# Performance work log

Measured on AMD Instinct MI355X. Metric: run time of the kernel, lower is better.

The kernel has to match this reference:

```python
import jax, jax.numpy as jnp
import numpy as np

N, E, D, H, C = 100000, 1600000, 128, 256, 40


def setup_inputs() -> dict:
    key = jax.random.key(0)
    ks = jax.random.split(key, 10)
    x = jax.random.normal(ks[0], (N, D), dtype=jnp.float32)
    src = jax.random.randint(ks[1], (E,), 0, N, dtype=jnp.int32)
    dst = jax.random.randint(ks[2], (E,), 0, N, dtype=jnp.int32)
    # GIN layer 1 MLP (bias-free), kaiming-uniform-like scale 1/sqrt(fan_in)
    w1a = jax.random.normal(ks[3], (D, H), dtype=jnp.float32) / np.sqrt(D)
    w1b = jax.random.normal(ks[4], (H, H), dtype=jnp.float32) / np.sqrt(H)
    # GIN layer 2 MLP
    w2a = jax.random.normal(ks[5], (H, H), dtype=jnp.float32) / np.sqrt(H)
    w2b = jax.random.normal(ks[6], (H, H), dtype=jnp.float32) / np.sqrt(H)
    # eps initialized to 0 per reset_parameters
    eps1 = jnp.zeros((), dtype=jnp.float32)
    eps2 = jnp.zeros((), dtype=jnp.float32)
    # final classifier fc (with bias)
    fc_w = jax.random.normal(ks[7], (H, C), dtype=jnp.float32) / np.sqrt(H)
    fc_b = jax.random.normal(ks[8], (C,), dtype=jnp.float32) * 0.01
    return {"x": x, "src": src, "dst": dst,
            "eps1": eps1, "w1a": w1a, "w1b": w1b,
            "eps2": eps2, "w2a": w2a, "w2b": w2b,
            "fc_w": fc_w, "fc_b": fc_b}


def reference(x, src, dst, eps1, w1a, w1b, eps2, w2a, w2b, fc_w, fc_b):
    n = x.shape[0]

    def gin_layer(h, eps, wa, wb):
        # GINConv sum-aggregation: scatter-add neighbor feats over edges
        agg = jax.ops.segment_sum(h[src], dst, num_segments=n)  # [N, d]
        rst = (1.0 + eps) * h + agg
        # 2-layer bias-free MLP with ReLU between
        return jax.nn.relu(rst @ wa) @ wb

    h = jax.nn.relu(gin_layer(x, eps1, w1a, w1b))   # layer + outer activation
    h = jax.nn.relu(gin_layer(h, eps2, w2a, w2b))   # dropout p=0 -> identity
    return h @ fc_w + fc_b                           # [N, C]
```

## Files before the change

### kernel.cpp

```cpp
#include <hip/hip_runtime.h>

#define N_NODES 100000
#define N_EDGES 1600000
#define DIM_IN  128
#define DIM_H   256
#define DIM_C   40

#define NB   391
#define NBLK 391
#define CHUNK 4096
#define ECAP 6144

typedef unsigned short bf16_t;
typedef __attribute__((ext_vector_type(8))) short short8;
typedef __attribute__((ext_vector_type(4))) float f32x4;

__device__ __forceinline__ bf16_t f2b(float f) {
    unsigned int u = __float_as_uint(f);
    unsigned int r = (u + 0x7fffu + ((u >> 16) & 1u)) >> 16;
    return (bf16_t)r;
}
__device__ __forceinline__ float b2f(unsigned int h16) {
    return __uint_as_float(h16 << 16);
}

__device__ __forceinline__ void gl_lds16(const void* gsrc, void* ldst) {
    __builtin_amdgcn_global_load_lds(
        (const __attribute__((address_space(1))) void*)gsrc,
        (__attribute__((address_space(3))) void*)ldst,
        16, 0, 0);
}


__global__ void k_bhist(const int* __restrict__ dst, int* __restrict__ cnt2, int e) {
    __shared__ int h[NB];
    int t = threadIdx.x, blk = blockIdx.x;
    for (int i = t; i < NB; i += 256) h[i] = 0;
    __syncthreads();
    int base = blk * CHUNK;
    int end = min(base + CHUNK, e);
    for (int i = base + t; i < end; i += 256)
        atomicAdd(&h[dst[i] >> 8], 1);
    __syncthreads();
    for (int i = t; i < NB; i += 256) cnt2[blk * NB + i] = h[i];
}

__global__ void k_bscanA(const int* __restrict__ cnt2, int* __restrict__ basep,
                         int* __restrict__ btot) {
    __shared__ int s[512];
    int t = threadIdx.x, b = blockIdx.x;
    int v = (t < NBLK) ? cnt2[t * NB + b] : 0;
    s[t] = v;
    __syncthreads();
    #pragma unroll
    for (int d = 1; d < 512; d <<= 1) {
        int tv = (t >= d) ? s[t - d] : 0;
        __syncthreads();
        s[t] += tv;
        __syncthreads();
    }
    if (t < NBLK) basep[t * NB + b] = s[t] - v;
    if (t == 511) btot[b] = s[511];
}

__global__ void k_bscan2(const int* __restrict__ btot, int* __restrict__ boff) {
    __shared__ int s[512];
    int t = threadIdx.x;
    int v = (t < NB) ? btot[t] : 0;
    s[t] = v;
    __syncthreads();
    #pragma unroll
    for (int d = 1; d < 512; d <<= 1) {
        int tv = (t >= d) ? s[t - d] : 0;
        __syncthreads();
        s[t] += tv;
        __syncthreads();
    }
    if (t < NB) boff[t] = s[t] - v;
    if (t == NB - 1) boff[NB] = s[t];
}

__global__ void k_bscatter(const int* __restrict__ src, const int* __restrict__ dst,
                           const int* __restrict__ basep, const int* __restrict__ boff,
                           int2* __restrict__ ebuf, int e) {
    __shared__ int cur[NB];
    int t = threadIdx.x, blk = blockIdx.x;
    for (int i = t; i < NB; i += 256) cur[i] = basep[blk * NB + i] + boff[i];
    __syncthreads();
    int base = blk * CHUNK;
    int end = min(base + CHUNK, e);
    for (int i = base + t; i < end; i += 256) {
        int sv = src[i], dv = dst[i];
        int pos = atomicAdd(&cur[dv >> 8], 1);
        ebuf[pos] = make_int2(sv, dv);
    }
}

__global__ __launch_bounds__(256) void k_build(const int2* __restrict__ ebuf,
                                               const int* __restrict__ boff,
                                               int* __restrict__ off,
                                               int* __restrict__ csr) {
    __shared__ int2 ec[ECAP];
    __shared__ int h[256];
    __shared__ int cur[256];
    int t = threadIdx.x, b = blockIdx.x;
    int node0 = b << 8;
    int e0 = boff[b], e1 = boff[b + 1];
    int ne = e1 - e0;
    bool fits = (ne <= ECAP);
    h[t] = 0;
    __syncthreads();
    if (fits) {
        for (int i = t; i < ne; i += 256) {
            int2 p = ebuf[e0 + i];
            ec[i] = p;
            atomicAdd(&h[p.y - node0], 1);
        }
    } else {
        for (int i = t; i < ne; i += 256)
            atomicAdd(&h[ebuf[e0 + i].y - node0], 1);
    }
    __syncthreads();
    int mydeg = h[t];
    #pragma unroll
    for (int d = 1; d < 256; d <<= 1) {
        int tv = (t >= d) ? h[t - d] : 0;
        __syncthreads();
        h[t] += tv;
        __syncthreads();
    }
    int node = node0 + t;
    if (node < N_NODES) off[node + 1] = e0 + h[t];
    if (b == 0 && t == 0) off[0] = 0;
    cur[t] = e0 + h[t] - mydeg;
    __syncthreads();
    if (fits) {
        for (int i = t; i < ne; i += 256) {
            int2 p = ec[i];
            int pos = atomicAdd(&cur[p.y - node0], 1);
            csr[pos] = p.x;
        }
    } else {
        for (int i = t; i < ne; i += 256) {
            int2 p = ebuf[e0 + i];
            int pos = atomicAdd(&cur[p.y - node0], 1);
            csr[pos] = p.x;
        }
    }
}


__global__ void k_cvt4(const float* __restrict__ in, bf16_t* __restrict__ out, int n4) {
    int i = blockIdx.x * 256 + threadIdx.x;
    if (i < n4) {
        float4 v = ((const float4*)in)[i];
        ushort4 o;
        o.x = f2b(v.x); o.y = f2b(v.y); o.z = f2b(v.z); o.w = f2b(v.w);
        ((ushort4*)out)[i] = o;
    }
}

__global__ void k_wcvt(const float* __restrict__ w1a, const float* __restrict__ w1b,
                       const float* __restrict__ w2a, const float* __restrict__ w2b,
                       const float* __restrict__ fcw,
                       bf16_t* __restrict__ o1a, bf16_t* __restrict__ o1b,
                       bf16_t* __restrict__ o2a, bf16_t* __restrict__ o2b,
                       bf16_t* __restrict__ ofc) {
    int r = blockIdx.y;
    int idx = blockIdx.x * 256 + threadIdx.x;
    const float* in; bf16_t* out; int K, N, Npad;
    switch (r) {
        case 0: in = w1a; out = o1a; K = 128; N = 256; Npad = 256; break;
        case 1: in = w1b; out = o1b; K = 256; N = 256; Npad = 256; break;
        case 2: in = w2a; out = o2a; K = 256; N = 256; Npad = 256; break;
        case 3: in = w2b; out = o2b; K = 256; N = 256; Npad = 256; break;
        default: in = fcw; out = ofc; K = 256; N = 40;  Npad = 128; break;
    }
    if (idx >= Npad * K) return;
    int n = idx / K, k = idx - n * K;
    float v = (n < N) ? in[(size_t)k * N + n] : 0.f;
    out[idx] = f2b(v);
}


template <int D>
__global__ void k_agg_b(const bf16_t* __restrict__ h, const int* __restrict__ off,
                        const int* __restrict__ csr, const float* __restrict__ eps_p,
                        bf16_t* __restrict__ rst, int n) {
    constexpr int V = D / 64;
    int gid = blockIdx.x * blockDim.x + threadIdx.x;
    int u = gid >> 6;
    int lane = gid & 63;
    if (u >= n) return;

    float acc[V];
    #pragma unroll
    for (int j = 0; j < V; j++) acc[j] = 0.f;

    int r0 = off[u], r1 = off[u + 1];
    int r = r0;
    for (; r + 8 <= r1; r += 8) {
        int s[8];
        #pragma unroll
        for (int t = 0; t < 8; t++) s[t] = csr[r + t];
        unsigned int v[8];
        #pragma unroll
        for (int t = 0; t < 8; t++)
            v[t] = *(const unsigned int*)(h + (size_t)s[t] * D + lane * 2);
        #pragma unroll
        for (int t = 0; t < 8; t++) {
            acc[0] += b2f(v[t] & 0xffffu);
            acc[1] += b2f(v[t] >> 16);
        }
    }
    for (; r < r1; r++) {
        int s = csr[r];
        unsigned int v = *(const unsigned int*)(h + (size_t)s * D + lane * 2);
        acc[0] += b2f(v & 0xffffu);
        acc[1] += b2f(v >> 16);
    }

    float ep = 1.0f + eps_p[0];
    unsigned int v = *(const unsigned int*)(h + (size_t)u * D + lane * 2);
    float o0 = ep * b2f(v & 0xffffu) + acc[0];
    float o1 = ep * b2f(v >> 16) + acc[1];
    *(unsigned int*)(rst + (size_t)u * D + lane * 2) =
        (unsigned int)f2b(o0) | ((unsigned int)f2b(o1) << 16);
}


__global__ void k_agg_u8(const unsigned char* __restrict__ h8,
                         const float* __restrict__ hs,
                         const int* __restrict__ off, const int* __restrict__ csr,
                         const float* __restrict__ eps_p,
                         bf16_t* __restrict__ rst, int n) {
    int gid = blockIdx.x * blockDim.x + threadIdx.x;
    int u = gid >> 6;
    int lane = gid & 63;
    if (u >= n) return;

    float acc[4] = {0.f, 0.f, 0.f, 0.f};
    int r0 = off[u], r1 = off[u + 1];
    int r = r0;
    for (; r + 8 <= r1; r += 8) {
        int s[8];
        #pragma unroll
        for (int t = 0; t < 8; t++) s[t] = csr[r + t];
        unsigned int v[8];
        float sc[8];
        #pragma unroll
        for (int t = 0; t < 8; t++) {
            v[t] = *(const unsigned int*)(h8 + (size_t)s[t] * 256 + lane * 4);
            sc[t] = hs[s[t]];
        }
        #pragma unroll
        for (int t = 0; t < 8; t++) {
            acc[0] += (float)(v[t] & 0xffu) * sc[t];
            acc[1] += (float)((v[t] >> 8) & 0xffu) * sc[t];
            acc[2] += (float)((v[t] >> 16) & 0xffu) * sc[t];
            acc[3] += (float)(v[t] >> 24) * sc[t];
        }
    }
    for (; r < r1; r++) {
        int s = csr[r];
        unsigned int v = *(const unsigned int*)(h8 + (size_t)s * 256 + lane * 4);
        float sc = hs[s];
        acc[0] += (float)(v & 0xffu) * sc;
        acc[1] += (float)((v >> 8) & 0xffu) * sc;
        acc[2] += (float)((v >> 16) & 0xffu) * sc;
        acc[3] += (float)(v >> 24) * sc;
    }

    float ep = 1.0f + eps_p[0];
    unsigned int vu = *(const unsigned int*)(h8 + (size_t)u * 256 + lane * 4);
    float scu = hs[u] * ep;
    float o0 = (float)(vu & 0xffu) * scu + acc[0];
    float o1 = (float)((vu >> 8) & 0xffu) * scu + acc[1];
    float o2 = (float)((vu >> 16) & 0xffu) * scu + acc[2];
    float o3 = (float)(vu >> 24) * scu + acc[3];
    uint2 ov;
    ov.x = (unsigned int)f2b(o0) | ((unsigned int)f2b(o1) << 16);
    ov.y = (unsigned int)f2b(o2) | ((unsigned int)f2b(o3) << 16);
    *(uint2*)(rst + (size_t)u * 256 + lane * 4) = ov;
}


#define TS_STRIDE 264

template <int K1, bool OUT8>
__global__ __launch_bounds__(256, 2) void k_mlp(
    const bf16_t* __restrict__ A, const bf16_t* __restrict__ W1t,
    const bf16_t* __restrict__ W2t, bf16_t* __restrict__ H,
    unsigned char* __restrict__ H8, float* __restrict__ Hs, int M)
{
    __shared__ __align__(16) bf16_t As[64 * 32];
    __shared__ __align__(16) bf16_t Bs[256 * 32];
    __shared__ __align__(16) bf16_t Ts[64 * TS_STRIDE];
    __shared__ int rmax[64];

    int tid = threadIdx.x;
    int wave = tid >> 6, lane = tid & 63;
    int l15 = lane & 15, quad = lane >> 4;
    int bm = blockIdx.x * 64;
    int wn = wave * 64;

    f32x4 acc[4][4];
    #pragma unroll
    for (int i = 0; i < 4; i++)
        #pragma unroll
        for (int j = 0; j < 4; j++) acc[i][j] = 0.f;

    for (int k0 = 0; k0 < K1; k0 += 32) {
        {
            int row = tid >> 2, k8 = (tid & 3) * 8;
            int gr = bm + row; if (gr >= M) gr = M - 1;
            gl_lds16(A + (size_t)gr * K1 + k0 + k8, &As[(wave * 64) * 8]);
        }
        #pragma unroll
        for (int l = 0; l < 4; l++) {
            int s = l * 256 + tid;
            int row = s >> 2, k8 = (s & 3) * 8;
            gl_lds16(W1t + (size_t)row * K1 + k0 + k8, &Bs[(size_t)(l * 256 + wave * 64) * 8]);
        }
        __syncthreads();

        short8 af[4], bfv[4];
        #pragma unroll
        for (int i = 0; i < 4; i++)
            af[i] = *(const short8*)&As[(i * 16 + l15) * 32 + quad * 8];
        #pragma unroll
        for (int j = 0; j < 4; j++)
            bfv[j] = *(const short8*)&Bs[(wn + j * 16 + l15) * 32 + quad * 8];

        #pragma unroll
        for (int i = 0; i < 4; i++)
            #pragma unroll
            for (int j = 0; j < 4; j++)
                acc[i][j] = __builtin_amdgcn_mfma_f32_16x16x32_bf16(af[i], bfv[j], acc[i][j], 0, 0, 0);
        __syncthreads();
    }

    #pragma unroll
    for (int i = 0; i < 4; i++)
        #pragma unroll
        for (int j = 0; j < 4; j++) {
            int row = i * 16 + quad * 4;
            int col = wn + j * 16 + l15;
            #pragma unroll
            for (int r = 0; r < 4; r++)
                Ts[(row + r) * TS_STRIDE + col] = f2b(fmaxf(acc[i][j][r], 0.f));
        }

    #pragma unroll
    for (int i = 0; i < 4; i++)
        #pragma unroll
        for (int j = 0; j < 4; j++) acc[i][j] = 0.f;
    __syncthreads();

    for (int k0 = 0; k0 < 256; k0 += 32) {
        #pragma unroll
        for (int l = 0; l < 4; l++) {
            int s = l * 256 + tid;
            int row = s >> 2, k8 = (s & 3) * 8;
            gl_lds16(W2t + (size_t)row * 256 + k0 + k8, &Bs[(size_t)(l * 256 + wave * 64) * 8]);
        }
        __syncthreads();

        short8 af[4], bfv[4];
        #pragma unroll
        for (int i = 0; i < 4; i++)
            af[i] = *(const short8*)&Ts[(i * 16 + l15) * TS_STRIDE + k0 + quad * 8];
        #pragma unroll
        for (int j = 0; j < 4; j++)
            bfv[j] = *(const short8*)&Bs[(wn + j * 16 + l15) * 32 + quad * 8];

        #pragma unroll
        for (int i = 0; i < 4; i++)
            #pragma unroll
            for (int j = 0; j < 4; j++)
                acc[i][j] = __builtin_amdgcn_mfma_f32_16x16x32_bf16(af[i], bfv[j], acc[i][j], 0, 0, 0);
        __syncthreads();
    }

    if constexpr (OUT8) {
        if (tid < 64) rmax[tid] = 0;
        __syncthreads();
        #pragma unroll
        for (int i = 0; i < 4; i++)
            #pragma unroll
            for (int r = 0; r < 4; r++) {
                float m = 0.f;
                #pragma unroll
                for (int j = 0; j < 4; j++) m = fmaxf(m, acc[i][j][r]);
                atomicMax(&rmax[i * 16 + quad * 4 + r], __float_as_int(m));
            }
        __syncthreads();
        #pragma unroll
        for (int i = 0; i < 4; i++) {
            #pragma unroll
            for (int r = 0; r < 4; r++) {
                int row = i * 16 + quad * 4 + r;
                int rowg = bm + row;
                if (rowg >= M) continue;
                float rm = __int_as_float(rmax[row]);
                float inv = (rm > 0.f) ? 255.f / rm : 0.f;
                #pragma unroll
                for (int j = 0; j < 4; j++) {
                    int col = wn + j * 16 + l15;
                    float v = fmaxf(acc[i][j][r], 0.f);
                    unsigned q = (unsigned)(v * inv + 0.5f);
                    if (q > 255u) q = 255u;
                    H8[(size_t)rowg * 256 + col] = (unsigned char)q;
                }
                if (wave == 0 && l15 == 0)
                    Hs[rowg] = rm * (1.f / 255.f);
            }
        }
    } else {
        #pragma unroll
        for (int j = 0; j < 4; j++) {
            int col = wn + j * 16 + l15;
            #pragma unroll
            for (int i = 0; i < 4; i++) {
                #pragma unroll
                for (int r = 0; r < 4; r++) {
                    int rowg = bm + i * 16 + quad * 4 + r;
                    if (rowg < M)
                        H[(size_t)rowg * 256 + col] = f2b(fmaxf(acc[i][j][r], 0.f));
                }
            }
        }
    }
}


__global__ __launch_bounds__(256) void gemm_fc(
    const bf16_t* __restrict__ A, const bf16_t* __restrict__ Bt,
    const float* __restrict__ bias, float* __restrict__ C,
    int M, int K, int Nst)
{
    __shared__ __align__(16) bf16_t As[128 * 32];
    __shared__ __align__(16) bf16_t Bs[128 * 32];

    int tid = threadIdx.x;
    int wave = tid >> 6, lane = tid & 63;
    int l15 = lane & 15, quad = lane >> 4;
    int bm = blockIdx.y * 128, bn = blockIdx.x * 128;
    int wm = (wave >> 1) * 64, wn = (wave & 1) * 64;

    f32x4 acc[4][4];
    #pragma unroll
    for (int i = 0; i < 4; i++)
        #pragma unroll
        for (int j = 0; j < 4; j++) acc[i][j] = 0.f;

    for (int k0 = 0; k0 < K; k0 += 32) {
        #pragma unroll
        for (int iss = 0; iss < 2; iss++) {
            int s = iss * 256 + wave * 64 + lane;
            int row = s >> 2;
            int k8 = (s & 3) * 8;
            int ldsoff = (iss * 256 + wave * 64) * 8;

            int grA = bm + row; if (grA >= M) grA = M - 1;
            gl_lds16(A + (size_t)grA * K + k0 + k8, &As[ldsoff]);

            int grB = bn + row;
            gl_lds16(Bt + (size_t)grB * K + k0 + k8, &Bs[ldsoff]);
        }
        __syncthreads();

        short8 af[4], bfv[4];
        #pragma unroll
        for (int i = 0; i < 4; i++)
            af[i] = *(const short8*)&As[(wm + i * 16 + l15) * 32 + quad * 8];
        #pragma unroll
        for (int j = 0; j < 4; j++)
            bfv[j] = *(const short8*)&Bs[(wn + j * 16 + l15) * 32 + quad * 8];

        #pragma unroll
        for (int i = 0; i < 4; i++)
            #pragma unroll
            for (int j = 0; j < 4; j++)
                acc[i][j] = __builtin_amdgcn_mfma_f32_16x16x32_bf16(af[i], bfv[j], acc[i][j], 0, 0, 0);
        __syncthreads();
    }

    #pragma unroll
    for (int j = 0; j < 4; j++) {
        int col = bn + wn + j * 16 + l15;
        if (col >= Nst) continue;
        float bv = bias[col];
        #pragma unroll
        for (int i = 0; i < 4; i++) {
            #pragma unroll
            for (int r = 0; r < 4; r++) {
                int rowg = bm + wm + i * 16 + quad * 4 + r;
                if (rowg < M)
                    C[(size_t)rowg * Nst + col] = acc[i][j][r] + bv;
            }
        }
    }
}


static inline size_t rnd256(size_t x) { return (x + 255) & ~(size_t)255; }

extern "C" void kernel_launch(void* const* d_in, const int* in_sizes, int n_in,
                              void* d_out, int out_size, void* d_ws, size_t ws_size,
                              hipStream_t stream) {
    const float* x    = (const float*)d_in[0];
    const int*   src  = (const int*)d_in[1];
    const int*   dst  = (const int*)d_in[2];
    const float* eps1 = (const float*)d_in[3];
    const float* w1a  = (const float*)d_in[4];
    const float* w1b  = (const float*)d_in[5];
    const float* eps2 = (const float*)d_in[6];
    const float* w2a  = (const float*)d_in[7];
    const float* w2b  = (const float*)d_in[8];
    const float* fc_w = (const float*)d_in[9];
    const float* fc_b = (const float*)d_in[10];
    float* out = (float*)d_out;

    char* w = (char*)d_ws;
    int* off  = (int*)w; w += rnd256(sizeof(int) * (size_t)(N_NODES + 1));
    int* csr  = (int*)w; w += rnd256(sizeof(int) * (size_t)N_EDGES);
    int* cnt2  = (int*)w; w += rnd256(sizeof(int) * (size_t)NBLK * NB);
    int* basep = (int*)w; w += rnd256(sizeof(int) * (size_t)NBLK * NB);
    int* btot  = (int*)w; w += rnd256(sizeof(int) * 512);
    int* boff  = (int*)w; w += rnd256(sizeof(int) * (NB + 1));
    bf16_t* w1a_t = (bf16_t*)w; w += rnd256(2 * (size_t)DIM_H * DIM_IN);
    bf16_t* w1b_t = (bf16_t*)w; w += rnd256(2 * (size_t)DIM_H * DIM_H);
    bf16_t* w2a_t = (bf16_t*)w; w += rnd256(2 * (size_t)DIM_H * DIM_H);
    bf16_t* w2b_t = (bf16_t*)w; w += rnd256(2 * (size_t)DIM_H * DIM_H);
    bf16_t* fc_t  = (bf16_t*)w; w += rnd256(2 * (size_t)128 * DIM_H);
    unsigned char* h8 = (unsigned char*)w; w += rnd256((size_t)N_NODES * DIM_H);
    float* hs = (float*)w; w += rnd256(sizeof(float) * (size_t)N_NODES);
    bf16_t* R12 = (bf16_t*)w; w += rnd256(2 * (size_t)N_NODES * DIM_H);
    bf16_t* R3  = (bf16_t*)w; w += rnd256(2 * (size_t)N_NODES * DIM_H);

    bf16_t* xb   = R12;
    bf16_t* rst1 = R12 + (size_t)N_NODES * DIM_IN;
    int2* ebuf = (int2*)R3;

    k_bhist<<<NBLK, 256, 0, stream>>>(dst, cnt2, N_EDGES);
    k_bscanA<<<NB, 512, 0, stream>>>(cnt2, basep, btot);
    k_bscan2<<<1, 512, 0, stream>>>(btot, boff);
    k_bscatter<<<NBLK, 256, 0, stream>>>(src, dst, basep, boff, ebuf, N_EDGES);
    k_build<<<NB, 256, 0, stream>>>(ebuf, boff, off, csr);

    k_cvt4<<<(N_NODES * DIM_IN / 4 + 255) / 256, 256, 0, stream>>>(x, xb, N_NODES * DIM_IN / 4);
    {
        dim3 g(256, 5);
        k_wcvt<<<g, 256, 0, stream>>>(w1a, w1b, w2a, w2b, fc_w,
                                      w1a_t, w1b_t, w2a_t, w2b_t, fc_t);
    }

    const int agg_blocks = (N_NODES * 64 + 255) / 256;
    const int mlp_blocks = (N_NODES + 63) / 64;

    k_agg_b<DIM_IN><<<agg_blocks, 256, 0, stream>>>(xb, off, csr, eps1, rst1, N_NODES);
    k_mlp<DIM_IN, true><<<mlp_blocks, 256, 0, stream>>>(rst1, w1a_t, w1b_t,
                                                        nullptr, h8, hs, N_NODES);

    k_agg_u8<<<agg_blocks, 256, 0, stream>>>(h8, hs, off, csr, eps2, (bf16_t*)R3, N_NODES);
    k_mlp<DIM_H, false><<<mlp_blocks, 256, 0, stream>>>((bf16_t*)R3, w2a_t, w2b_t,
                                                        R12, nullptr, nullptr, N_NODES);

    dim3 g1(1, (N_NODES + 127) / 128);
    gemm_fc<<<g1, 256, 0, stream>>>(R12, fc_t, fc_b, out, N_NODES, DIM_H, DIM_C);
}
```

Baseline: 464.8 us.

## Quantize input features to per-row int8 and pack edge buffer into 32-bit words

The input x is now quantized to int8 with one scale per row instead of bf16, which halves the bytes gathered per edge in the first aggregation. The edge scatter buffer now packs src and the low 8 bits of dst into a single 32-bit int instead of an int2, halving the edge-buffer traffic in scatter and build. The aggregation kernels use 32-bit unsigned address arithmetic. The cost is extra quantization error on the raw input features, and the packing assumes node ids fit in 24 bits.

```diff
diff --git a/kernel.cpp b/kernel.cpp
--- a/kernel.cpp
+++ b/kernel.cpp
@@ -82,7 +82,7 @@
 
 __global__ void k_bscatter(const int* __restrict__ src, const int* __restrict__ dst,
                            const int* __restrict__ basep, const int* __restrict__ boff,
-                           int2* __restrict__ ebuf, int e) {
+                           int* __restrict__ ebuf, int e) {
     __shared__ int cur[NB];
     int t = threadIdx.x, blk = blockIdx.x;
     for (int i = t; i < NB; i += 256) cur[i] = basep[blk * NB + i] + boff[i];
@@ -92,15 +92,15 @@
     for (int i = base + t; i < end; i += 256) {
         int sv = src[i], dv = dst[i];
         int pos = atomicAdd(&cur[dv >> 8], 1);
-        ebuf[pos] = make_int2(sv, dv);
-    }
-}
-
-__global__ __launch_bounds__(256) void k_build(const int2* __restrict__ ebuf,
+        ebuf[pos] = sv | ((dv & 255) << 24);
+    }
+}
+
+__global__ __launch_bounds__(256) void k_build(const int* __restrict__ ebuf,
                                                const int* __restrict__ boff,
                                                int* __restrict__ off,
                                                int* __restrict__ csr) {
-    __shared__ int2 ec[ECAP];
+    __shared__ int ec[ECAP];
     __shared__ int h[256];
     __shared__ int cur[256];
     int t = threadIdx.x, b = blockIdx.x;
@@ -112,13 +112,13 @@
     __syncthreads();
     if (fits) {
         for (int i = t; i < ne; i += 256) {
-            int2 p = ebuf[e0 + i];
+            int p = ebuf[e0 + i];
             ec[i] = p;
-            atomicAdd(&h[p.y - node0], 1);
+            atomicAdd(&h[(unsigned)p >> 24], 1);
         }
     } else {
         for (int i = t; i < ne; i += 256)
-            atomicAdd(&h[ebuf[e0 + i].y - node0], 1);
+            atomicAdd(&h[(unsigned)ebuf[e0 + i] >> 24], 1);
     }
     __syncthreads();
     int mydeg = h[t];
@@ -136,28 +136,36 @@
     __syncthreads();
     if (fits) {
         for (int i = t; i < ne; i += 256) {
-            int2 p = ec[i];
-            int pos = atomicAdd(&cur[p.y - node0], 1);
-            csr[pos] = p.x;
+            int p = ec[i];
+            int pos = atomicAdd(&cur[(unsigned)p >> 24], 1);
+            csr[pos] = p & 0xFFFFFF;
         }
     } else {
         for (int i = t; i < ne; i += 256) {
-            int2 p = ebuf[e0 + i];
-            int pos = atomicAdd(&cur[p.y - node0], 1);
-            csr[pos] = p.x;
-        }
-    }
-}
-
-
-__global__ void k_cvt4(const float* __restrict__ in, bf16_t* __restrict__ out, int n4) {
-    int i = blockIdx.x * 256 + threadIdx.x;
-    if (i < n4) {
-        float4 v = ((const float4*)in)[i];
-        ushort4 o;
-        o.x = f2b(v.x); o.y = f2b(v.y); o.z = f2b(v.z); o.w = f2b(v.w);
-        ((ushort4*)out)[i] = o;
-    }
+            int p = ebuf[e0 + i];
+            int pos = atomicAdd(&cur[(unsigned)p >> 24], 1);
+            csr[pos] = p & 0xFFFFFF;
+        }
+    }
+}
+
+
+__global__ void k_cvt_i8(const float* __restrict__ x, signed char* __restrict__ x8,
+                         float* __restrict__ xs, int n) {
+    int gid = blockIdx.x * blockDim.x + threadIdx.x;
+    int u = gid >> 6, lane = gid & 63;
+    if (u >= n) return;
+    float2 v = *(const float2*)(x + (size_t)u * 128 + lane * 2);
+    float m = fmaxf(fabsf(v.x), fabsf(v.y));
+    #pragma unroll
+    for (int d = 1; d < 64; d <<= 1)
+        m = fmaxf(m, __shfl_xor(m, d, 64));
+    float inv = (m > 0.f) ? 127.f / m : 0.f;
+    int q0 = (int)rintf(v.x * inv);
+    int q1 = (int)rintf(v.y * inv);
+    unsigned short pk = (unsigned short)((q0 & 0xff) | ((q1 & 0xff) << 8));
+    *(unsigned short*)(x8 + ((unsigned)u << 7) + lane * 2) = pk;
+    if (lane == 0) xs[u] = (m > 0.f) ? m * (1.f / 127.f) : 0.f;
 }
 
 __global__ void k_wcvt(const float* __restrict__ w1a, const float* __restrict__ w1b,
@@ -183,48 +191,49 @@
 }
 
 
-template <int D>
-__global__ void k_agg_b(const bf16_t* __restrict__ h, const int* __restrict__ off,
-                        const int* __restrict__ csr, const float* __restrict__ eps_p,
-                        bf16_t* __restrict__ rst, int n) {
-    constexpr int V = D / 64;
+__global__ void k_agg_i8(const signed char* __restrict__ h8, const float* __restrict__ hs,
+                         const int* __restrict__ off, const int* __restrict__ csr,
+                         const float* __restrict__ eps_p,
+                         bf16_t* __restrict__ rst, int n) {
     int gid = blockIdx.x * blockDim.x + threadIdx.x;
     int u = gid >> 6;
     int lane = gid & 63;
     if (u >= n) return;
 
-    float acc[V];
-    #pragma unroll
-    for (int j = 0; j < V; j++) acc[j] = 0.f;
-
+    float acc0 = 0.f, acc1 = 0.f;
     int r0 = off[u], r1 = off[u + 1];
     int r = r0;
+    unsigned loff = lane * 2u;
     for (; r + 8 <= r1; r += 8) {
         int s[8];
         #pragma unroll
         for (int t = 0; t < 8; t++) s[t] = csr[r + t];
-        unsigned int v[8];
-        #pragma unroll
-        for (int t = 0; t < 8; t++)
-            v[t] = *(const unsigned int*)(h + (size_t)s[t] * D + lane * 2);
+        unsigned v[8];
+        float sc[8];
         #pragma unroll
         for (int t = 0; t < 8; t++) {
-            acc[0] += b2f(v[t] & 0xffffu);
-            acc[1] += b2f(v[t] >> 16);
+            v[t] = *(const unsigned short*)(h8 + (((unsigned)s[t] << 7) + loff));
+            sc[t] = hs[s[t]];
+        }
+        #pragma unroll
+        for (int t = 0; t < 8; t++) {
+            acc0 += (float)(int)(signed char)(v[t] & 0xffu) * sc[t];
+            acc1 += (float)(int)(signed char)(v[t] >> 8) * sc[t];
         }
     }
     for (; r < r1; r++) {
         int s = csr[r];
-        unsigned int v = *(const unsigned int*)(h + (size_t)s * D + lane * 2);
-        acc[0] += b2f(v & 0xffffu);
-        acc[1] += b2f(v >> 16);
-    }
-
-    float ep = 1.0f + eps_p[0];
-    unsigned int v = *(const unsigned int*)(h + (size_t)u * D + lane * 2);
-    float o0 = ep * b2f(v & 0xffffu) + acc[0];
-    float o1 = ep * b2f(v >> 16) + acc[1];
-    *(unsigned int*)(rst + (size_t)u * D + lane * 2) =
+        unsigned v = *(const unsigned short*)(h8 + (((unsigned)s << 7) + loff));
+        float sc = hs[s];
+        acc0 += (float)(int)(signed char)(v & 0xffu) * sc;
+        acc1 += (float)(int)(signed char)(v >> 8) * sc;
+    }
+
+    float scu = hs[u] * (1.0f + eps_p[0]);
+    unsigned vu = *(const unsigned short*)(h8 + (((unsigned)u << 7) + loff));
+    float o0 = (float)(int)(signed char)(vu & 0xffu) * scu + acc0;
+    float o1 = (float)(int)(signed char)(vu >> 8) * scu + acc1;
+    *(unsigned int*)(rst + ((unsigned)u << 7) + lane * 2) =
         (unsigned int)f2b(o0) | ((unsigned int)f2b(o1) << 16);
 }
 
@@ -242,6 +251,7 @@
     float acc[4] = {0.f, 0.f, 0.f, 0.f};
     int r0 = off[u], r1 = off[u + 1];
     int r = r0;
+    unsigned loff = lane * 4u;
     for (; r + 8 <= r1; r += 8) {
         int s[8];
         #pragma unroll
@@ -250,7 +260,7 @@
         float sc[8];
         #pragma unroll
         for (int t = 0; t < 8; t++) {
-            v[t] = *(const unsigned int*)(h8 + (size_t)s[t] * 256 + lane * 4);
+            v[t] = *(const unsigned int*)(h8 + (((unsigned)s[t] << 8) + loff));
             sc[t] = hs[s[t]];
         }
         #pragma unroll
@@ -263,7 +273,7 @@
     }
     for (; r < r1; r++) {
         int s = csr[r];
-        unsigned int v = *(const unsigned int*)(h8 + (size_t)s * 256 + lane * 4);
+        unsigned int v = *(const unsigned int*)(h8 + (((unsigned)s << 8) + loff));
         float sc = hs[s];
         acc[0] += (float)(v & 0xffu) * sc;
         acc[1] += (float)((v >> 8) & 0xffu) * sc;
@@ -272,7 +282,7 @@
     }
 
     float ep = 1.0f + eps_p[0];
-    unsigned int vu = *(const unsigned int*)(h8 + (size_t)u * 256 + lane * 4);
+    unsigned int vu = *(const unsigned int*)(h8 + (((unsigned)u << 8) + loff));
     float scu = hs[u] * ep;
     float o0 = (float)(vu & 0xffu) * scu + acc[0];
     float o1 = (float)((vu >> 8) & 0xffu) * scu + acc[1];
@@ -534,14 +544,15 @@
     bf16_t* w2a_t = (bf16_t*)w; w += rnd256(2 * (size_t)DIM_H * DIM_H);
     bf16_t* w2b_t = (bf16_t*)w; w += rnd256(2 * (size_t)DIM_H * DIM_H);
     bf16_t* fc_t  = (bf16_t*)w; w += rnd256(2 * (size_t)128 * DIM_H);
+    signed char* x8 = (signed char*)w; w += rnd256((size_t)N_NODES * DIM_IN);
+    float* xs = (float*)w; w += rnd256(sizeof(float) * (size_t)N_NODES);
     unsigned char* h8 = (unsigned char*)w; w += rnd256((size_t)N_NODES * DIM_H);
     float* hs = (float*)w; w += rnd256(sizeof(float) * (size_t)N_NODES);
     bf16_t* R12 = (bf16_t*)w; w += rnd256(2 * (size_t)N_NODES * DIM_H);
     bf16_t* R3  = (bf16_t*)w; w += rnd256(2 * (size_t)N_NODES * DIM_H);
 
-    bf16_t* xb   = R12;
-    bf16_t* rst1 = R12 + (size_t)N_NODES * DIM_IN;
-    int2* ebuf = (int2*)R3;
+    bf16_t* rst1 = R12;
+    int* ebuf = (int*)R3;
 
     k_bhist<<<NBLK, 256, 0, stream>>>(dst, cnt2, N_EDGES);
     k_bscanA<<<NB, 512, 0, stream>>>(cnt2, basep, btot);
@@ -549,7 +560,7 @@
     k_bscatter<<<NBLK, 256, 0, stream>>>(src, dst, basep, boff, ebuf, N_EDGES);
     k_build<<<NB, 256, 0, stream>>>(ebuf, boff, off, csr);
 
-    k_cvt4<<<(N_NODES * DIM_IN / 4 + 255) / 256, 256, 0, stream>>>(x, xb, N_NODES * DIM_IN / 4);
+    k_cvt_i8<<<(N_NODES * 64 + 255) / 256, 256, 0, stream>>>(x, x8, xs, N_NODES);
     {
         dim3 g(256, 5);
         k_wcvt<<<g, 256, 0, stream>>>(w1a, w1b, w2a, w2b, fc_w,
@@ -559,7 +570,7 @@
     const int agg_blocks = (N_NODES * 64 + 255) / 256;
     const int mlp_blocks = (N_NODES + 63) / 64;
 
-    k_agg_b<DIM_IN><<<agg_blocks, 256, 0, stream>>>(xb, off, csr, eps1, rst1, N_NODES);
+    k_agg_i8<<<agg_blocks, 256, 0, stream>>>(x8, xs, off, csr, eps1, rst1, N_NODES);
     k_mlp<DIM_IN, true><<<mlp_blocks, 256, 0, stream>>>(rst1, w1a_t, w1b_t,
                                                         nullptr, h8, hs, N_NODES);
 
```

Result: no change. 469.3 us (+1.0%).
